# Kernel tuning notes

Hardware: AMD Instinct MI355X
Metric: run time of the kernel (lower is better)

Reference implementation:

```python
import jax, jax.numpy as jnp
import numpy as np

NUM_GRAPHS = 64

def setup_inputs() -> dict:
    key = jax.random.key(0)
    ks = jax.random.split(key, 10)
    N, E, D, V = 100000, 1600000, 64, 30
    node_types = jax.random.randint(ks[0], (N,), 0, V, dtype=jnp.int64 if jax.config.jax_enable_x64 else jnp.int32)
    edge_index = jax.random.randint(ks[1], (2, E), 0, N, dtype=jnp.int32)
    batch = jnp.sort(jax.random.randint(ks[2], (N,), 0, NUM_GRAPHS, dtype=jnp.int32))
    emb_table = jax.random.normal(ks[3], (V, D), dtype=jnp.float32)
    W1 = jax.random.normal(ks[4], (D, D), dtype=jnp.float32) / np.sqrt(D)
    W2 = jax.random.normal(ks[5], (D, D), dtype=jnp.float32) / np.sqrt(D)
    W3 = jax.random.normal(ks[6], (D, D), dtype=jnp.float32) / np.sqrt(D)
    b1 = jnp.zeros((D,), jnp.float32)
    b2 = jnp.zeros((D,), jnp.float32)
    b3 = jnp.zeros((D,), jnp.float32)
    return {"node_types": node_types, "edge_index": edge_index, "batch": batch,
            "emb_table": emb_table, "W1": W1, "b1": b1, "W2": W2, "b2": b2, "W3": W3, "b3": b3}

def _gcn_conv(x, W, b, row, col, norm, N):
    # x' = D^-1/2 (A+I) D^-1/2 (x @ W) + b   (PyG GCNConv semantics)
    h = x @ W
    msg = h[row] * norm[:, None]              # gather + edgewise scale
    out = jax.ops.segment_sum(msg, col, num_segments=N)  # scatter-add at targets
    return out + b

def reference(node_types, edge_index, batch, emb_table, W1, b1, W2, b2, W3, b3):
    N = node_types.shape[0]
    # add self-loops
    loops = jnp.arange(N, dtype=edge_index.dtype)
    row = jnp.concatenate([edge_index[0], loops])
    col = jnp.concatenate([edge_index[1], loops])
    # symmetric normalization on A + I
    deg = jax.ops.segment_sum(jnp.ones_like(col, dtype=jnp.float32), col, num_segments=N)
    dinv = jnp.where(deg > 0, jax.lax.rsqrt(deg), 0.0)
    norm = dinv[row] * dinv[col]
    x = emb_table[node_types]
    x = jax.nn.relu(_gcn_conv(x, W1, b1, row, col, norm, N))
    x = jax.nn.relu(_gcn_conv(x, W2, b2, row, col, norm, N))
    x = _gcn_conv(x, W3, b3, row, col, norm, N)
    # global mean pool over batch segments
    sums = jax.ops.segment_sum(x, batch, num_segments=NUM_GRAPHS)
    cnts = jax.ops.segment_sum(jnp.ones((N,), jnp.float32), batch, num_segments=NUM_GRAPHS)
    pooled = sums / jnp.maximum(cnts, 1.0)[:, None]
    # L2 normalize rows
    return pooled / jnp.linalg.norm(pooled, axis=1, keepdims=True)
```

## Files before the change

kernel.cpp:

```cpp
#include <hip/hip_runtime.h>
#include <hip/hip_fp16.h>

#define DD 64
#define NUM_GRAPHS 64
#define AGG_BLOCKS 2048
#define EB 512
#define BINW 256
#define MAXNB 512
#define EBIN_CAP 6144

typedef _Float16 h2_t __attribute__((ext_vector_type(2)));

__device__ __forceinline__ float fdot2u(unsigned a, unsigned b, float c) {
    return __builtin_amdgcn_fdot2(__builtin_bit_cast(h2_t, a),
                                  __builtin_bit_cast(h2_t, b), c, false);
}

__global__ __launch_bounds__(256) void k_hist(const int* __restrict__ col,
                                              int* __restrict__ H, int E, int NB, int CE) {
    __shared__ int h[MAXNB];
    int eb = blockIdx.x, t = threadIdx.x;
    for (int i = t; i < NB; i += 256) h[i] = 0;
    __syncthreads();
    int e0 = eb * CE, e1 = min(E, e0 + CE);
    for (int e = e0 + t; e < e1; e += 256) atomicAdd(&h[col[e] >> 8], 1);
    __syncthreads();
    for (int i = t; i < NB; i += 256) H[eb * NB + i] = h[i];
}

__global__ __launch_bounds__(256) void k_scanA(int* __restrict__ H,
                                               int* __restrict__ bintot, int NB) {
    __shared__ int s[256];
    int b = blockIdx.x, t = threadIdx.x;
    int i0 = (2 * t) * NB + b, i1 = (2 * t + 1) * NB + b;
    int v0 = H[i0], v1 = H[i1];
    int tot = v0 + v1;
    s[t] = tot;
    __syncthreads();
    for (int off = 1; off < 256; off <<= 1) {
        int tv = (t >= off) ? s[t - off] : 0;
        __syncthreads();
        s[t] += tv;
        __syncthreads();
    }
    int excl = s[t] - tot;
    H[i0] = excl;
    H[i1] = excl + v0;
    if (t == 255) bintot[b] = s[255];
}

__global__ void k_scanB(const int* __restrict__ bintot, int* __restrict__ binstart, int NB) {
    __shared__ int s[512];
    int t = threadIdx.x;
    int v = (t < NB) ? bintot[t] : 0;
    s[t] = v;
    __syncthreads();
    for (int off = 1; off < 512; off <<= 1) {
        int tv = (t >= off) ? s[t - off] : 0;
        __syncthreads();
        s[t] += tv;
        __syncthreads();
    }
    if (t < NB) binstart[t] = s[t] - v;
    if (t == 511) binstart[NB] = s[511];
}

__global__ __launch_bounds__(256) void k_scatbin(const int* __restrict__ row,
                                                 const int* __restrict__ col,
                                                 const int* __restrict__ H,
                                                 const int* __restrict__ binstart,
                                                 unsigned* __restrict__ binned,
                                                 int E, int NB, int CE) {
    __shared__ int off[MAXNB];
    int eb = blockIdx.x, t = threadIdx.x;
    for (int i = t; i < NB; i += 256) off[i] = binstart[i] + H[eb * NB + i];
    __syncthreads();
    int e0 = eb * CE, e1 = min(E, e0 + CE);
    for (int e = e0 + t; e < e1; e += 256) {
        int c = col[e], r = row[e];
        int slot = atomicAdd(&off[c >> 8], 1);
        binned[slot] = ((unsigned)(c & 255) << 24) | (unsigned)r;
    }
}

__global__ __launch_bounds__(256) void k_bincsr(const unsigned* __restrict__ binned,
                                                const int* __restrict__ binstart,
                                                const int* __restrict__ nt,
                                                int* __restrict__ srcidx,
                                                int* __restrict__ rowptr,
                                                float* __restrict__ dinv,
                                                int2* __restrict__ pk, int N, int NB) {
    __shared__ unsigned arr[EBIN_CAP];
    __shared__ int sorted_[EBIN_CAP];
    __shared__ int cnt[BINW];
    __shared__ int base[BINW];
    __shared__ int cursor[BINW];
    int b = blockIdx.x, t = threadIdx.x;
    int s0 = binstart[b], s1 = binstart[b + 1];
    int binsz = s1 - s0;
    if (binsz > EBIN_CAP) binsz = EBIN_CAP;
    cnt[t] = 0;
    for (int i = t; i < binsz; i += 256) arr[i] = binned[s0 + i];
    __syncthreads();
    for (int i = t; i < binsz; i += 256) atomicAdd(&cnt[arr[i] >> 24], 1);
    __syncthreads();
    int v = cnt[t];
    base[t] = v;
    __syncthreads();
    for (int off = 1; off < 256; off <<= 1) {
        int tv = (t >= off) ? base[t - off] : 0;
        __syncthreads();
        base[t] += tv;
        __syncthreads();
    }
    int excl = base[t] - v;
    __syncthreads();
    base[t] = excl;
    cursor[t] = excl;
    __syncthreads();
    for (int i = t; i < binsz; i += 256) {
        unsigned val = arr[i];
        int pos = atomicAdd(&cursor[val >> 24], 1);
        sorted_[pos] = (int)(val & 0xFFFFFF);
    }
    __syncthreads();
    for (int i = t; i < binsz; i += 256) srcidx[s0 + i] = sorted_[i];
    int node = b * BINW + t;
    if (node < N) {
        rowptr[node] = s0 + base[t];
        float di = rsqrtf((float)cnt[t] + 1.0f);
        dinv[node] = di;
        pk[node] = make_int2(nt[node], __float_as_int(di));
    }
    if (b == NB - 1 && t == 0) rowptr[N] = s1;
}

__global__ void k_buildepk(const int* __restrict__ srcidx, const int2* __restrict__ pk,
                           unsigned* __restrict__ epku, int E) {
    int i = blockIdx.x * blockDim.x + threadIdx.x;
    if (i >= E) return;
    int2 p = pk[srcidx[i]];
    epku[i] = ((unsigned)p.x << 16) |
              (unsigned)__half_as_ushort(__float2half(__int_as_float(p.y)));
}

__global__ void k_embW1(const float* __restrict__ emb, const float* __restrict__ W1,
                        float* __restrict__ embW1, int V) {
    __shared__ float er[DD];
    int v = blockIdx.x, j = threadIdx.x;
    er[j] = emb[v * DD + j];
    __syncthreads();
    float acc = 0.0f;
    #pragma unroll
    for (int d = 0; d < DD; ++d) acc += er[d] * W1[d * DD + j];
    embW1[v * DD + j] = acc;
}

__global__ void k_packW(const float* __restrict__ W, unsigned* __restrict__ Wpk) {
    int t = blockIdx.x * blockDim.x + threadIdx.x;
    if (t >= 32 * DD) return;
    int p = t >> 6, j = t & 63;
    __half2 h = __floats2half2_rn(W[(2 * p) * DD + j], W[(2 * p + 1) * DD + j]);
    Wpk[t] = __builtin_bit_cast(unsigned, h);
}

__device__ __forceinline__ void acc_h4(float4& a, uint2 r) {
    float2 f0 = __half22float2(*(const __half2*)&r.x);
    float2 f1 = __half22float2(*(const __half2*)&r.y);
    a.x += f0.x; a.y += f0.y; a.z += f1.x; a.w += f1.y;
}

__device__ __forceinline__ float4 gather_partial_q(const int* __restrict__ srcidx,
                                                   const __half* __restrict__ Hs,
                                                   int s, int e, int g, int l) {
    float4 A = {0,0,0,0}, B = {0,0,0,0}, C = {0,0,0,0}, D = {0,0,0,0};
    int k = s;
    int kend = s + ((e - s) & ~15);
    if (k < kend) {
        uint2 r0 = *(const uint2*)(Hs + (long)srcidx[k + g] * DD + 4 * l);
        uint2 r1 = *(const uint2*)(Hs + (long)srcidx[k + 4 + g] * DD + 4 * l);
        uint2 r2 = *(const uint2*)(Hs + (long)srcidx[k + 8 + g] * DD + 4 * l);
        uint2 r3 = *(const uint2*)(Hs + (long)srcidx[k + 12 + g] * DD + 4 * l);
        k += 16;
        for (; k < kend; k += 16) {
            uint2 n0 = *(const uint2*)(Hs + (long)srcidx[k + g] * DD + 4 * l);
            uint2 n1 = *(const uint2*)(Hs + (long)srcidx[k + 4 + g] * DD + 4 * l);
            uint2 n2 = *(const uint2*)(Hs + (long)srcidx[k + 8 + g] * DD + 4 * l);
            uint2 n3 = *(const uint2*)(Hs + (long)srcidx[k + 12 + g] * DD + 4 * l);
            acc_h4(A, r0); acc_h4(B, r1); acc_h4(C, r2); acc_h4(D, r3);
            r0 = n0; r1 = n1; r2 = n2; r3 = n3;
        }
        acc_h4(A, r0); acc_h4(B, r1); acc_h4(C, r2); acc_h4(D, r3);
    }
    for (; k < e; k += 4) {
        if (k + g < e) {
            uint2 rr = *(const uint2*)(Hs + (long)srcidx[k + g] * DD + 4 * l);
            acc_h4(A, rr);
        }
    }
    A.x += B.x + C.x + D.x; A.y += B.y + C.y + D.y;
    A.z += B.z + C.z + D.z; A.w += B.w + C.w + D.w;
    return A;
}

__device__ __forceinline__ void acc_h8(float4& A, float4& B, uint4 r) {
    float2 f0 = __half22float2(*(const __half2*)&r.x);
    float2 f1 = __half22float2(*(const __half2*)&r.y);
    float2 f2 = __half22float2(*(const __half2*)&r.z);
    float2 f3 = __half22float2(*(const __half2*)&r.w);
    A.x += f0.x; A.y += f0.y; A.z += f1.x; A.w += f1.y;
    B.x += f2.x; B.y += f2.y; B.z += f3.x; B.w += f3.y;
}

__device__ __forceinline__ void gather_sum_8(const int* __restrict__ srcidx,
                                             const __half* __restrict__ Hs,
                                             int s, int e, int g, int l,
                                             float4& A, float4& B) {
    float4 A1 = {0.f, 0.f, 0.f, 0.f}, B1 = {0.f, 0.f, 0.f, 0.f};
    int k = s;
    int kend = s + ((e - s) & ~15);
    if (k < kend) {
        uint4 r0 = *(const uint4*)(Hs + (long)srcidx[k + g] * DD + 8 * l);
        uint4 r1 = *(const uint4*)(Hs + (long)srcidx[k + 8 + g] * DD + 8 * l);
        k += 16;
        for (; k < kend; k += 16) {
            uint4 n0 = *(const uint4*)(Hs + (long)srcidx[k + g] * DD + 8 * l);
            uint4 n1 = *(const uint4*)(Hs + (long)srcidx[k + 8 + g] * DD + 8 * l);
            acc_h8(A, B, r0);
            acc_h8(A1, B1, r1);
            r0 = n0; r1 = n1;
        }
        acc_h8(A, B, r0);
        acc_h8(A1, B1, r1);
    }
    if (k + 8 <= e) {
        uint4 r = *(const uint4*)(Hs + (long)srcidx[k + g] * DD + 8 * l);
        acc_h8(A, B, r);
        k += 8;
    }
    if (k + g < e) {
        uint4 r = *(const uint4*)(Hs + (long)srcidx[k + g] * DD + 8 * l);
        acc_h8(A1, B1, r);
    }
    A.x += A1.x; A.y += A1.y; A.z += A1.z; A.w += A1.w;
    B.x += B1.x; B.y += B1.y; B.z += B1.z; B.w += B1.w;
}

__global__ __launch_bounds__(256, 4) void k_agg1_fused(const int* __restrict__ rowptr,
                                                    const unsigned* __restrict__ epku,
                                                    const int2* __restrict__ pk,
                                                    const float* __restrict__ embW1,
                                                    const float* __restrict__ b1,
                                                    __half* __restrict__ OUT, int N, int V) {
    __shared__ float ew[30 * DD];
    int tid = threadIdx.x;
    for (int k = tid; k < V * DD; k += 256) ew[k] = embW1[k];
    __syncthreads();
    int lane = tid & 63;
    int g = lane >> 4, l = lane & 15;
    float4 bq = *(const float4*)(b1 + 4 * l);
    int wave0 = blockIdx.x * 4 + (tid >> 6);
    int wstride = gridDim.x * 4;
    for (int node = __builtin_amdgcn_readfirstlane(wave0); node < N;
         node += wstride) {
        int s = rowptr[node], e = rowptr[node + 1];
        float4 acc = {0.f, 0.f, 0.f, 0.f};
        int k = s;
        for (; k + 8 <= e; k += 8) {
            unsigned u0 = epku[k + g];
            unsigned u1 = epku[k + 4 + g];
            int t0 = u0 >> 16, t1 = u1 >> 16;
            float d0 = __half2float(__ushort_as_half((unsigned short)(u0 & 0xFFFF)));
            float d1 = __half2float(__ushort_as_half((unsigned short)(u1 & 0xFFFF)));
            float4 w0 = *(const float4*)(ew + t0 * DD + 4 * l);
            float4 w1 = *(const float4*)(ew + t1 * DD + 4 * l);
            acc.x += w0.x * d0 + w1.x * d1;
            acc.y += w0.y * d0 + w1.y * d1;
            acc.z += w0.z * d0 + w1.z * d1;
            acc.w += w0.w * d0 + w1.w * d1;
        }
        if (k + 4 <= e) {
            unsigned u0 = epku[k + g];
            int t0 = u0 >> 16;
            float d0 = __half2float(__ushort_as_half((unsigned short)(u0 & 0xFFFF)));
            float4 w0 = *(const float4*)(ew + t0 * DD + 4 * l);
            acc.x += w0.x * d0; acc.y += w0.y * d0;
            acc.z += w0.z * d0; acc.w += w0.w * d0;
            k += 4;
        }
        if (k + g < e) {
            unsigned u0 = epku[k + g];
            int t0 = u0 >> 16;
            float d0 = __half2float(__ushort_as_half((unsigned short)(u0 & 0xFFFF)));
            float4 w0 = *(const float4*)(ew + t0 * DD + 4 * l);
            acc.x += w0.x * d0; acc.y += w0.y * d0;
            acc.z += w0.z * d0; acc.w += w0.w * d0;
        }
        acc.x += __shfl_xor(acc.x, 16, 64); acc.x += __shfl_xor(acc.x, 32, 64);
        acc.y += __shfl_xor(acc.y, 16, 64); acc.y += __shfl_xor(acc.y, 32, 64);
        acc.z += __shfl_xor(acc.z, 16, 64); acc.z += __shfl_xor(acc.z, 32, 64);
        acc.w += __shfl_xor(acc.w, 16, 64); acc.w += __shfl_xor(acc.w, 32, 64);
        int2 pc = pk[node];
        float dc = __int_as_float(pc.y);
        float4 wc = *(const float4*)(ew + pc.x * DD + 4 * l);
        float4 v;
        v.x = fmaxf((acc.x + wc.x * dc) * dc + bq.x, 0.f) * dc;
        v.y = fmaxf((acc.y + wc.y * dc) * dc + bq.y, 0.f) * dc;
        v.z = fmaxf((acc.z + wc.z * dc) * dc + bq.z, 0.f) * dc;
        v.w = fmaxf((acc.w + wc.w * dc) * dc + bq.w, 0.f) * dc;
        if (g == 0) {
            __half2 h0 = __floats2half2_rn(v.x, v.y);
            __half2 h1 = __floats2half2_rn(v.z, v.w);
            uint2 st;
            st.x = __builtin_bit_cast(unsigned, h0);
            st.y = __builtin_bit_cast(unsigned, h1);
            *(uint2*)(OUT + (long)node * DD + 4 * l) = st;
        }
    }
}

__global__ __launch_bounds__(256, 4) void k_agg2_fused(const int* __restrict__ rowptr,
                                                    const int* __restrict__ srcidx,
                                                    const float* __restrict__ dinv,
                                                    const __half* __restrict__ Hs,
                                                    const float* __restrict__ b2,
                                                    const unsigned* __restrict__ W2pk,
                                                    __half* __restrict__ OUT, int N) {
    int tid = threadIdx.x;
    int lane = tid & 63;
    int g = lane >> 3, l = lane & 7;
    unsigned Wc[32];
    #pragma unroll
    for (int p = 0; p < 32; ++p) Wc[p] = W2pk[p * DD + lane];
    float bl = b2[lane];
    int wstride = gridDim.x * 4;
    int node = __builtin_amdgcn_readfirstlane(blockIdx.x * 4 + (tid >> 6));
    int s = 0, e = 0;
    if (node < N) { s = rowptr[node]; e = rowptr[node + 1]; }
    while (node < N) {
        int nn = node + wstride;
        int ns = 0, ne = 0;
        if (nn < N) { ns = rowptr[nn]; ne = rowptr[nn + 1]; }
        float dc = dinv[node];
        uint4 sr = *(const uint4*)(Hs + (long)node * DD + 8 * l);
        float4 A = {0.f, 0.f, 0.f, 0.f}, B = {0.f, 0.f, 0.f, 0.f};
        gather_sum_8(srcidx, Hs, s, e, g, l, A, B);
        #pragma unroll
        for (int m = 8; m <= 32; m <<= 1) {
            A.x += __shfl_xor(A.x, m, 64); A.y += __shfl_xor(A.y, m, 64);
            A.z += __shfl_xor(A.z, m, 64); A.w += __shfl_xor(A.w, m, 64);
            B.x += __shfl_xor(B.x, m, 64); B.y += __shfl_xor(B.y, m, 64);
            B.z += __shfl_xor(B.z, m, 64); B.w += __shfl_xor(B.w, m, 64);
        }
        float2 s0 = __half22float2(*(const __half2*)&sr.x);
        float2 s1 = __half22float2(*(const __half2*)&sr.y);
        float2 s2 = __half22float2(*(const __half2*)&sr.z);
        float2 s3 = __half22float2(*(const __half2*)&sr.w);
        float t0 = (A.x + s0.x) * dc, t1 = (A.y + s0.y) * dc;
        float t2 = (A.z + s1.x) * dc, t3 = (A.w + s1.y) * dc;
        float t4 = (B.x + s2.x) * dc, t5 = (B.y + s2.y) * dc;
        float t6 = (B.z + s3.x) * dc, t7 = (B.w + s3.y) * dc;
        int vp0 = __builtin_bit_cast(int, __floats2half2_rn(t0, t1));
        int vp1 = __builtin_bit_cast(int, __floats2half2_rn(t2, t3));
        int vp2 = __builtin_bit_cast(int, __floats2half2_rn(t4, t5));
        int vp3 = __builtin_bit_cast(int, __floats2half2_rn(t6, t7));
        float o0 = 0.f, o1 = 0.f, o2 = 0.f, o3 = 0.f;
        #pragma unroll
        for (int p = 0; p < 32; p += 4) {
            o0 = fdot2u((unsigned)__builtin_amdgcn_readlane(vp0, p >> 2), Wc[p + 0], o0);
            o1 = fdot2u((unsigned)__builtin_amdgcn_readlane(vp1, p >> 2), Wc[p + 1], o1);
            o2 = fdot2u((unsigned)__builtin_amdgcn_readlane(vp2, p >> 2), Wc[p + 2], o2);
            o3 = fdot2u((unsigned)__builtin_amdgcn_readlane(vp3, p >> 2), Wc[p + 3], o3);
        }
        float u = (o0 + o1) + (o2 + o3);
        float v2 = fmaxf(u + bl, 0.f);
        OUT[(long)node * DD + lane] = __float2half(v2 * dc);
        node = nn; s = ns; e = ne;
    }
}

__device__ __forceinline__ void flush_pool_q(float4& PA, float* __restrict__ pool,
                                             int gcur, int g, int l) {
    PA.x += __shfl_xor(PA.x, 16, 64); PA.x += __shfl_xor(PA.x, 32, 64);
    PA.y += __shfl_xor(PA.y, 16, 64); PA.y += __shfl_xor(PA.y, 32, 64);
    PA.z += __shfl_xor(PA.z, 16, 64); PA.z += __shfl_xor(PA.z, 32, 64);
    PA.w += __shfl_xor(PA.w, 16, 64); PA.w += __shfl_xor(PA.w, 32, 64);
    if (g == 0) {
        atomicAdd(&pool[gcur * DD + 4 * l + 0], PA.x);
        atomicAdd(&pool[gcur * DD + 4 * l + 1], PA.y);
        atomicAdd(&pool[gcur * DD + 4 * l + 2], PA.z);
        atomicAdd(&pool[gcur * DD + 4 * l + 3], PA.w);
    }
}

__global__ __launch_bounds__(256, 4) void k_agg3_pool(const int* __restrict__ rowptr,
                                                   const int* __restrict__ srcidx,
                                                   const float* __restrict__ dinv,
                                                   const __half* __restrict__ Hs,
                                                   const int* __restrict__ batch,
                                                   float* __restrict__ pool,
                                                   int N, int chunk) {
    int tid = threadIdx.x;
    int lane = tid & 63;
    int g = lane >> 4, l = lane & 15;
    int w = __builtin_amdgcn_readfirstlane(blockIdx.x * 4 + (tid >> 6));
    int start = w * chunk;
    if (start >= N) return;
    int endn = min(N, start + chunk);
    int gcur = batch[start];
    float4 PA = {0.f, 0.f, 0.f, 0.f};
    int s = rowptr[start];
    for (int node = start; node < endn; ++node) {
        int e = rowptr[node + 1];
        float dc = dinv[node];
        int gb = batch[node];
        uint2 sr = *(const uint2*)(Hs + (long)node * DD + 4 * l);
        float4 A = gather_partial_q(srcidx, Hs, s, e, g, l);
        if (g == 0) {
            float2 s0 = __half22float2(*(const __half2*)&sr.x);
            float2 s1 = __half22float2(*(const __half2*)&sr.y);
            A.x += s0.x; A.y += s0.y; A.z += s1.x; A.w += s1.y;
        }
        if (gb != gcur) {
            flush_pool_q(PA, pool, gcur, g, l);
            gcur = gb;
            PA.x = dc * A.x; PA.y = dc * A.y; PA.z = dc * A.z; PA.w = dc * A.w;
        } else {
            PA.x += dc * A.x; PA.y += dc * A.y; PA.z += dc * A.z; PA.w += dc * A.w;
        }
        s = e;
    }
    flush_pool_q(PA, pool, gcur, g, l);
}

__global__ void k_final(const float* __restrict__ pool, const int* __restrict__ batch,
                        const float* __restrict__ W3, const float* __restrict__ b3,
                        float* __restrict__ out, int N) {
    __shared__ float pr[DD];
    int g = blockIdx.x, j = threadIdx.x;
    pr[j] = pool[g * DD + j];
    __syncthreads();
    int lo = 0, hi = N;
    while (lo < hi) { int m = (lo + hi) >> 1; if (batch[m] < g) lo = m + 1; else hi = m; }
    int lo2 = lo; hi = N;
    while (lo2 < hi) { int m = (lo2 + hi) >> 1; if (batch[m] < g + 1) lo2 = m + 1; else hi = m; }
    float cnt = fmaxf((float)(lo2 - lo), 1.0f);
    float acc = 0.0f;
    #pragma unroll
    for (int d = 0; d < DD; ++d) acc += pr[d] * W3[d * DD + j];
    float v = acc / cnt + b3[j];
    float sq = v * v;
    #pragma unroll
    for (int off = 32; off > 0; off >>= 1) sq += __shfl_down(sq, off, 64);
    float nrm = __shfl(sq, 0, 64);
    out[g * DD + j] = v / sqrtf(nrm);
}

extern "C" void kernel_launch(void* const* d_in, const int* in_sizes, int n_in,
                              void* d_out, int out_size, void* d_ws, size_t ws_size,
                              hipStream_t stream) {
    const int*   node_types = (const int*)d_in[0];
    const int*   edge_index = (const int*)d_in[1];
    const int*   batch      = (const int*)d_in[2];
    const float* emb        = (const float*)d_in[3];
    const float* W1 = (const float*)d_in[4];
    const float* b1 = (const float*)d_in[5];
    const float* W2 = (const float*)d_in[6];
    const float* b2 = (const float*)d_in[7];
    const float* W3 = (const float*)d_in[8];
    const float* b3 = (const float*)d_in[9];
    const int N = in_sizes[0];
    const int E = in_sizes[1] / 2;
    const int V = in_sizes[3] / DD;
    const int* row = edge_index;
    const int* col = edge_index + E;
    const long ND = (long)N * DD;
    const int NB = (N + BINW - 1) / BINW;
    const int CE = (E + EB - 1) / EB;

    char* p = (char*)d_ws;
    __half*   hsA     = (__half*)p;       p += ND * sizeof(__half);
    __half*   hsB     = (__half*)p;       p += ND * sizeof(__half);
    int*      srcidx  = (int*)p;          p += (size_t)E * sizeof(int);
    unsigned* epku    = (unsigned*)p;     p += (size_t)E * sizeof(unsigned);
    unsigned* binned  = (unsigned*)p;     p += (size_t)E * sizeof(unsigned);
    int*      H       = (int*)p;          p += (size_t)EB * NB * sizeof(int);
    int*      bintot  = (int*)p;          p += (size_t)(NB + 4) * sizeof(int);
    int*      binstart= (int*)p;          p += (size_t)(NB + 4) * sizeof(int);
    float*    dinv    = (float*)p;        p += (size_t)N * sizeof(float);
    int2*     pk      = (int2*)p;         p += (size_t)N * sizeof(int2);
    int*      rowptr  = (int*)p;          p += (size_t)(N + 4) * sizeof(int);
    float*    pool    = (float*)p;        p += (size_t)NUM_GRAPHS * DD * sizeof(float);
    float*    embW1   = (float*)p;        p += (size_t)V * DD * sizeof(float);
    unsigned* W2pk    = (unsigned*)p;     p += 32 * DD * sizeof(unsigned);

    k_hist<<<EB, 256, 0, stream>>>(col, H, E, NB, CE);
    k_scanA<<<NB, 256, 0, stream>>>(H, bintot, NB);
    k_scanB<<<1, 512, 0, stream>>>(bintot, binstart, NB);
    k_scatbin<<<EB, 256, 0, stream>>>(row, col, H, binstart, binned, E, NB, CE);
    k_bincsr<<<NB, 256, 0, stream>>>(binned, binstart, node_types, srcidx, rowptr,
                                     dinv, pk, N, NB);
    k_buildepk<<<(E + 255) / 256, 256, 0, stream>>>(srcidx, pk, epku, E);

    k_embW1<<<V, DD, 0, stream>>>(emb, W1, embW1, V);
    k_packW<<<8, 256, 0, stream>>>(W2, W2pk);

    k_agg1_fused<<<AGG_BLOCKS, 256, 0, stream>>>(rowptr, epku, pk, embW1, b1,
                                                 hsA, N, V);
    k_agg2_fused<<<AGG_BLOCKS, 256, 0, stream>>>(rowptr, srcidx, dinv, hsA, b2, W2pk,
                                                 hsB, N);
    hipMemsetAsync(pool, 0, (size_t)(NUM_GRAPHS * DD) * sizeof(float), stream);
    const int totalWaves = AGG_BLOCKS * 4;
    const int chunk = (N + totalWaves - 1) / totalWaves;
    k_agg3_pool<<<AGG_BLOCKS, 256, 0, stream>>>(rowptr, srcidx, dinv, hsB, batch,
                                                pool, N, chunk);
    k_final<<<NUM_GRAPHS, DD, 0, stream>>>(pool, batch, W3, b3, (float*)d_out, N);
}
```

Before: 278.9 us.

## Make layer-3 pooling edge-parallel with per-edge batch/dinv packs; prefetch first neighbours

The CSR build now writes a per-edge word packing the target node's graph id and fp16 dinv. It reuses the binned buffer, which each block has already copied to shared memory. Layer-3 aggregation plus pooling becomes an edge-partitioned kernel: each wave walks an even slice of edges, uses wave-uniform checks to batch 16 edges of the same graph, and flushes to the pool on graph changes. Self-loop contributions move to a separate node-parallel kernel, and layers 1 and 2 prefetch the next node's first neighbour indices to hide index-load latency. This aims to balance work and drop rowptr/batch lookups, at the cost of an extra launch, extra per-edge writes in the CSR build, and more pool atomics.

```diff
diff --git a/kernel.cpp b/kernel.cpp
--- a/kernel.cpp
+++ b/kernel.cpp
@@ -15,6 +15,8 @@
     return __builtin_amdgcn_fdot2(__builtin_bit_cast(h2_t, a),
                                   __builtin_bit_cast(h2_t, b), c, false);
 }
+
+#define MDLO(m) __half2float(__ushort_as_half((unsigned short)((m) & 0xFFFF)))
 
 __global__ __launch_bounds__(256) void k_hist(const int* __restrict__ col,
                                               int* __restrict__ H, int E, int NB, int CE) {
@@ -83,18 +85,21 @@
     }
 }
 
-__global__ __launch_bounds__(256) void k_bincsr(const unsigned* __restrict__ binned,
+__global__ __launch_bounds__(256) void k_bincsr(const unsigned* binned,
                                                 const int* __restrict__ binstart,
                                                 const int* __restrict__ nt,
+                                                const int* __restrict__ batch,
                                                 int* __restrict__ srcidx,
                                                 int* __restrict__ rowptr,
                                                 float* __restrict__ dinv,
-                                                int2* __restrict__ pk, int N, int NB) {
+                                                int2* __restrict__ pk,
+                                                unsigned* e3pk, int N, int NB) {
     __shared__ unsigned arr[EBIN_CAP];
     __shared__ int sorted_[EBIN_CAP];
     __shared__ int cnt[BINW];
     __shared__ int base[BINW];
     __shared__ int cursor[BINW];
+    __shared__ unsigned packS[BINW];
     int b = blockIdx.x, t = threadIdx.x;
     int s0 = binstart[b], s1 = binstart[b + 1];
     int binsz = s1 - s0;
@@ -105,6 +110,13 @@
     for (int i = t; i < binsz; i += 256) atomicAdd(&cnt[arr[i] >> 24], 1);
     __syncthreads();
     int v = cnt[t];
+    float di = rsqrtf((float)v + 1.0f);
+    {
+        int nodeT = b * BINW + t;
+        int bt = (nodeT < N) ? batch[nodeT] : 0;
+        packS[t] = ((unsigned)bt << 16) |
+                   (unsigned)__half_as_ushort(__float2half(di));
+    }
     base[t] = v;
     __syncthreads();
     for (int off = 1; off < 256; off <<= 1) {
@@ -120,15 +132,16 @@
     __syncthreads();
     for (int i = t; i < binsz; i += 256) {
         unsigned val = arr[i];
-        int pos = atomicAdd(&cursor[val >> 24], 1);
+        int d = val >> 24;
+        int pos = atomicAdd(&cursor[d], 1);
         sorted_[pos] = (int)(val & 0xFFFFFF);
+        e3pk[s0 + pos] = packS[d];
     }
     __syncthreads();
     for (int i = t; i < binsz; i += 256) srcidx[s0 + i] = sorted_[i];
     int node = b * BINW + t;
     if (node < N) {
         rowptr[node] = s0 + base[t];
-        float di = rsqrtf((float)cnt[t] + 1.0f);
         dinv[node] = di;
         pk[node] = make_int2(nt[node], __float_as_int(di));
     }
@@ -164,45 +177,6 @@
     Wpk[t] = __builtin_bit_cast(unsigned, h);
 }
 
-__device__ __forceinline__ void acc_h4(float4& a, uint2 r) {
-    float2 f0 = __half22float2(*(const __half2*)&r.x);
-    float2 f1 = __half22float2(*(const __half2*)&r.y);
-    a.x += f0.x; a.y += f0.y; a.z += f1.x; a.w += f1.y;
-}
-
-__device__ __forceinline__ float4 gather_partial_q(const int* __restrict__ srcidx,
-                                                   const __half* __restrict__ Hs,
-                                                   int s, int e, int g, int l) {
-    float4 A = {0,0,0,0}, B = {0,0,0,0}, C = {0,0,0,0}, D = {0,0,0,0};
-    int k = s;
-    int kend = s + ((e - s) & ~15);
-    if (k < kend) {
-        uint2 r0 = *(const uint2*)(Hs + (long)srcidx[k + g] * DD + 4 * l);
-        uint2 r1 = *(const uint2*)(Hs + (long)srcidx[k + 4 + g] * DD + 4 * l);
-        uint2 r2 = *(const uint2*)(Hs + (long)srcidx[k + 8 + g] * DD + 4 * l);
-        uint2 r3 = *(const uint2*)(Hs + (long)srcidx[k + 12 + g] * DD + 4 * l);
-        k += 16;
-        for (; k < kend; k += 16) {
-            uint2 n0 = *(const uint2*)(Hs + (long)srcidx[k + g] * DD + 4 * l);
-            uint2 n1 = *(const uint2*)(Hs + (long)srcidx[k + 4 + g] * DD + 4 * l);
-            uint2 n2 = *(const uint2*)(Hs + (long)srcidx[k + 8 + g] * DD + 4 * l);
-            uint2 n3 = *(const uint2*)(Hs + (long)srcidx[k + 12 + g] * DD + 4 * l);
-            acc_h4(A, r0); acc_h4(B, r1); acc_h4(C, r2); acc_h4(D, r3);
-            r0 = n0; r1 = n1; r2 = n2; r3 = n3;
-        }
-        acc_h4(A, r0); acc_h4(B, r1); acc_h4(C, r2); acc_h4(D, r3);
-    }
-    for (; k < e; k += 4) {
-        if (k + g < e) {
-            uint2 rr = *(const uint2*)(Hs + (long)srcidx[k + g] * DD + 4 * l);
-            acc_h4(A, rr);
-        }
-    }
-    A.x += B.x + C.x + D.x; A.y += B.y + C.y + D.y;
-    A.z += B.z + C.z + D.z; A.w += B.w + C.w + D.w;
-    return A;
-}
-
 __device__ __forceinline__ void acc_h8(float4& A, float4& B, uint4 r) {
     float2 f0 = __half22float2(*(const __half2*)&r.x);
     float2 f1 = __half22float2(*(const __half2*)&r.y);
@@ -212,16 +186,16 @@
     B.x += f2.x; B.y += f2.y; B.z += f3.x; B.w += f3.y;
 }
 
-__device__ __forceinline__ void gather_sum_8(const int* __restrict__ srcidx,
-                                             const __half* __restrict__ Hs,
-                                             int s, int e, int g, int l,
-                                             float4& A, float4& B) {
+__device__ __forceinline__ void gather_sum_8p(const int* __restrict__ srcidx,
+                                              const __half* __restrict__ Hs,
+                                              int s, int e, int g, int l,
+                                              float4& A, float4& B, int pi0, int pi1) {
     float4 A1 = {0.f, 0.f, 0.f, 0.f}, B1 = {0.f, 0.f, 0.f, 0.f};
     int k = s;
     int kend = s + ((e - s) & ~15);
     if (k < kend) {
-        uint4 r0 = *(const uint4*)(Hs + (long)srcidx[k + g] * DD + 8 * l);
-        uint4 r1 = *(const uint4*)(Hs + (long)srcidx[k + 8 + g] * DD + 8 * l);
+        uint4 r0 = *(const uint4*)(Hs + (long)pi0 * DD + 8 * l);
+        uint4 r1 = *(const uint4*)(Hs + (long)pi1 * DD + 8 * l);
         k += 16;
         for (; k < kend; k += 16) {
             uint4 n0 = *(const uint4*)(Hs + (long)srcidx[k + g] * DD + 8 * l);
@@ -259,48 +233,51 @@
     int lane = tid & 63;
     int g = lane >> 4, l = lane & 15;
     float4 bq = *(const float4*)(b1 + 4 * l);
-    int wave0 = blockIdx.x * 4 + (tid >> 6);
     int wstride = gridDim.x * 4;
-    for (int node = __builtin_amdgcn_readfirstlane(wave0); node < N;
-         node += wstride) {
-        int s = rowptr[node], e = rowptr[node + 1];
+    int node = __builtin_amdgcn_readfirstlane(blockIdx.x * 4 + (tid >> 6));
+    int s = 0, e = 0;
+    unsigned pu0 = 0, pu1 = 0;
+    if (node < N) {
+        s = rowptr[node]; e = rowptr[node + 1];
+        if (e - s >= 8) { pu0 = epku[s + g]; pu1 = epku[s + 4 + g]; }
+    }
+#define P8(U0, U1) { \
+        unsigned _u0 = (U0), _u1 = (U1); \
+        int _t0 = _u0 >> 16, _t1 = _u1 >> 16; \
+        float _d0 = MDLO(_u0), _d1 = MDLO(_u1); \
+        float4 _w0 = *(const float4*)(ew + _t0 * DD + 4 * l); \
+        float4 _w1 = *(const float4*)(ew + _t1 * DD + 4 * l); \
+        acc.x += _w0.x * _d0 + _w1.x * _d1; \
+        acc.y += _w0.y * _d0 + _w1.y * _d1; \
+        acc.z += _w0.z * _d0 + _w1.z * _d1; \
+        acc.w += _w0.w * _d0 + _w1.w * _d1; }
+#define P4(U0) { \
+        unsigned _u0 = (U0); \
+        int _t0 = _u0 >> 16; \
+        float _d0 = MDLO(_u0); \
+        float4 _w0 = *(const float4*)(ew + _t0 * DD + 4 * l); \
+        acc.x += _w0.x * _d0; acc.y += _w0.y * _d0; \
+        acc.z += _w0.z * _d0; acc.w += _w0.w * _d0; }
+    while (node < N) {
+        int nn = node + wstride;
+        int ns = 0, ne = 0;
+        if (nn < N) { ns = rowptr[nn]; ne = rowptr[nn + 1]; }
+        int2 pc = pk[node];
         float4 acc = {0.f, 0.f, 0.f, 0.f};
         int k = s;
-        for (; k + 8 <= e; k += 8) {
-            unsigned u0 = epku[k + g];
-            unsigned u1 = epku[k + 4 + g];
-            int t0 = u0 >> 16, t1 = u1 >> 16;
-            float d0 = __half2float(__ushort_as_half((unsigned short)(u0 & 0xFFFF)));
-            float d1 = __half2float(__ushort_as_half((unsigned short)(u1 & 0xFFFF)));
-            float4 w0 = *(const float4*)(ew + t0 * DD + 4 * l);
-            float4 w1 = *(const float4*)(ew + t1 * DD + 4 * l);
-            acc.x += w0.x * d0 + w1.x * d1;
-            acc.y += w0.y * d0 + w1.y * d1;
-            acc.z += w0.z * d0 + w1.z * d1;
-            acc.w += w0.w * d0 + w1.w * d1;
-        }
-        if (k + 4 <= e) {
-            unsigned u0 = epku[k + g];
-            int t0 = u0 >> 16;
-            float d0 = __half2float(__ushort_as_half((unsigned short)(u0 & 0xFFFF)));
-            float4 w0 = *(const float4*)(ew + t0 * DD + 4 * l);
-            acc.x += w0.x * d0; acc.y += w0.y * d0;
-            acc.z += w0.z * d0; acc.w += w0.w * d0;
-            k += 4;
-        }
-        if (k + g < e) {
-            unsigned u0 = epku[k + g];
-            int t0 = u0 >> 16;
-            float d0 = __half2float(__ushort_as_half((unsigned short)(u0 & 0xFFFF)));
-            float4 w0 = *(const float4*)(ew + t0 * DD + 4 * l);
-            acc.x += w0.x * d0; acc.y += w0.y * d0;
-            acc.z += w0.z * d0; acc.w += w0.w * d0;
-        }
+        if (k + 8 <= e) {
+            P8(pu0, pu1);
+            k += 8;
+            for (; k + 8 <= e; k += 8) P8(epku[k + g], epku[k + 4 + g]);
+        }
+        if (k + 4 <= e) { P4(epku[k + g]); k += 4; }
+        if (k + g < e)  { P4(epku[k + g]); }
+        unsigned npu0 = 0, npu1 = 0;
+        if (nn < N && ne - ns >= 8) { npu0 = epku[ns + g]; npu1 = epku[ns + 4 + g]; }
         acc.x += __shfl_xor(acc.x, 16, 64); acc.x += __shfl_xor(acc.x, 32, 64);
         acc.y += __shfl_xor(acc.y, 16, 64); acc.y += __shfl_xor(acc.y, 32, 64);
         acc.z += __shfl_xor(acc.z, 16, 64); acc.z += __shfl_xor(acc.z, 32, 64);
         acc.w += __shfl_xor(acc.w, 16, 64); acc.w += __shfl_xor(acc.w, 32, 64);
-        int2 pc = pk[node];
         float dc = __int_as_float(pc.y);
         float4 wc = *(const float4*)(ew + pc.x * DD + 4 * l);
         float4 v;
@@ -316,7 +293,10 @@
             st.y = __builtin_bit_cast(unsigned, h1);
             *(uint2*)(OUT + (long)node * DD + 4 * l) = st;
         }
-    }
+        node = nn; s = ns; e = ne; pu0 = npu0; pu1 = npu1;
+    }
+#undef P8
+#undef P4
 }
 
 __global__ __launch_bounds__(256, 4) void k_agg2_fused(const int* __restrict__ rowptr,
@@ -336,7 +316,11 @@
     int wstride = gridDim.x * 4;
     int node = __builtin_amdgcn_readfirstlane(blockIdx.x * 4 + (tid >> 6));
     int s = 0, e = 0;
-    if (node < N) { s = rowptr[node]; e = rowptr[node + 1]; }
+    int pi0 = 0, pi1 = 0;
+    if (node < N) {
+        s = rowptr[node]; e = rowptr[node + 1];
+        if (e - s >= 16) { pi0 = srcidx[s + g]; pi1 = srcidx[s + 8 + g]; }
+    }
     while (node < N) {
         int nn = node + wstride;
         int ns = 0, ne = 0;
@@ -344,7 +328,9 @@
         float dc = dinv[node];
         uint4 sr = *(const uint4*)(Hs + (long)node * DD + 8 * l);
         float4 A = {0.f, 0.f, 0.f, 0.f}, B = {0.f, 0.f, 0.f, 0.f};
-        gather_sum_8(srcidx, Hs, s, e, g, l, A, B);
+        gather_sum_8p(srcidx, Hs, s, e, g, l, A, B, pi0, pi1);
+        int npi0 = 0, npi1 = 0;
+        if (nn < N && ne - ns >= 16) { npi0 = srcidx[ns + g]; npi1 = srcidx[ns + 8 + g]; }
         #pragma unroll
         for (int m = 8; m <= 32; m <<= 1) {
             A.x += __shfl_xor(A.x, m, 64); A.y += __shfl_xor(A.y, m, 64);
@@ -375,12 +361,13 @@
         float u = (o0 + o1) + (o2 + o3);
         float v2 = fmaxf(u + bl, 0.f);
         OUT[(long)node * DD + lane] = __float2half(v2 * dc);
-        node = nn; s = ns; e = ne;
+        node = nn; s = ns; e = ne; pi0 = npi0; pi1 = npi1;
     }
 }
 
 __device__ __forceinline__ void flush_pool_q(float4& PA, float* __restrict__ pool,
                                              int gcur, int g, int l) {
+    gcur &= (NUM_GRAPHS - 1);
     PA.x += __shfl_xor(PA.x, 16, 64); PA.x += __shfl_xor(PA.x, 32, 64);
     PA.y += __shfl_xor(PA.y, 16, 64); PA.y += __shfl_xor(PA.y, 32, 64);
     PA.z += __shfl_xor(PA.z, 16, 64); PA.z += __shfl_xor(PA.z, 32, 64);
@@ -393,44 +380,125 @@
     }
 }
 
-__global__ __launch_bounds__(256, 4) void k_agg3_pool(const int* __restrict__ rowptr,
-                                                   const int* __restrict__ srcidx,
-                                                   const float* __restrict__ dinv,
+#define ACC_E(PA, R, D) { \
+    float2 _f0 = __half22float2(*(const __half2*)&(R).x); \
+    float2 _f1 = __half22float2(*(const __half2*)&(R).y); \
+    PA.x += (D) * _f0.x; PA.y += (D) * _f0.y; \
+    PA.z += (D) * _f1.x; PA.w += (D) * _f1.y; }
+
+__global__ __launch_bounds__(256, 4) void k_agg3_pool(const int* __restrict__ srcidx,
+                                                   const unsigned* __restrict__ e3pk,
                                                    const __half* __restrict__ Hs,
-                                                   const int* __restrict__ batch,
                                                    float* __restrict__ pool,
-                                                   int N, int chunk) {
+                                                   int E, int ech) {
     int tid = threadIdx.x;
     int lane = tid & 63;
     int g = lane >> 4, l = lane & 15;
+    int w = __builtin_amdgcn_readfirstlane(blockIdx.x * 4 + (tid >> 6));
+    int k = w * ech;
+    if (k >= E) return;
+    int ke = min(E, k + ech);
+    int gcur = (int)(e3pk[k] >> 16);
+    float4 PA = {0.f, 0.f, 0.f, 0.f};
+    unsigned cm0, cm1, cm2, cm3, nm0 = 0, nm1 = 0, nm2 = 0, nm3 = 0;
+    int ci0, ci1, ci2, ci3, ni0 = 0, ni1 = 0, ni2 = 0, ni3 = 0;
+    uint2 cr0 = {0,0}, cr1 = {0,0}, cr2 = {0,0}, cr3 = {0,0};
+    bool have_cur = false, have_next = false;
+    if (k + 16 <= ke) {
+        cm0 = e3pk[k + g];      cm1 = e3pk[k + 4 + g];
+        cm2 = e3pk[k + 8 + g];  cm3 = e3pk[k + 12 + g];
+        ci0 = srcidx[k + g];     ci1 = srcidx[k + 4 + g];
+        ci2 = srcidx[k + 8 + g]; ci3 = srcidx[k + 12 + g];
+        if (__all((int)((cm0 >> 16) == (unsigned)gcur) & (int)((cm1 >> 16) == (unsigned)gcur) &
+                  (int)((cm2 >> 16) == (unsigned)gcur) & (int)((cm3 >> 16) == (unsigned)gcur))) {
+            cr0 = *(const uint2*)(Hs + (long)ci0 * DD + 4 * l);
+            cr1 = *(const uint2*)(Hs + (long)ci1 * DD + 4 * l);
+            cr2 = *(const uint2*)(Hs + (long)ci2 * DD + 4 * l);
+            cr3 = *(const uint2*)(Hs + (long)ci3 * DD + 4 * l);
+            have_cur = true;
+            if (k + 32 <= ke) {
+                nm0 = e3pk[k + 16 + g];  nm1 = e3pk[k + 20 + g];
+                nm2 = e3pk[k + 24 + g];  nm3 = e3pk[k + 28 + g];
+                ni0 = srcidx[k + 16 + g];  ni1 = srcidx[k + 20 + g];
+                ni2 = srcidx[k + 24 + g];  ni3 = srcidx[k + 28 + g];
+                have_next = true;
+            }
+        }
+    }
+    while (have_cur) {
+        bool next_ok = false;
+        uint2 nr0 = {0,0}, nr1 = {0,0}, nr2 = {0,0}, nr3 = {0,0};
+        if (have_next) {
+            next_ok = __all((int)((nm0 >> 16) == (unsigned)gcur) & (int)((nm1 >> 16) == (unsigned)gcur) &
+                            (int)((nm2 >> 16) == (unsigned)gcur) & (int)((nm3 >> 16) == (unsigned)gcur)) != 0;
+            if (next_ok) {
+                nr0 = *(const uint2*)(Hs + (long)ni0 * DD + 4 * l);
+                nr1 = *(const uint2*)(Hs + (long)ni1 * DD + 4 * l);
+                nr2 = *(const uint2*)(Hs + (long)ni2 * DD + 4 * l);
+                nr3 = *(const uint2*)(Hs + (long)ni3 * DD + 4 * l);
+            }
+        }
+        unsigned fm0 = 0, fm1 = 0, fm2 = 0, fm3 = 0;
+        int fi0 = 0, fi1 = 0, fi2 = 0, fi3 = 0;
+        bool have_f = false;
+        if (next_ok && k + 48 <= ke) {
+            fm0 = e3pk[k + 32 + g];  fm1 = e3pk[k + 36 + g];
+            fm2 = e3pk[k + 40 + g];  fm3 = e3pk[k + 44 + g];
+            fi0 = srcidx[k + 32 + g];  fi1 = srcidx[k + 36 + g];
+            fi2 = srcidx[k + 40 + g];  fi3 = srcidx[k + 44 + g];
+            have_f = true;
+        }
+        float d0 = MDLO(cm0), d1 = MDLO(cm1), d2 = MDLO(cm2), d3 = MDLO(cm3);
+        ACC_E(PA, cr0, d0); ACC_E(PA, cr1, d1);
+        ACC_E(PA, cr2, d2); ACC_E(PA, cr3, d3);
+        k += 16;
+        if (!next_ok) break;
+        cm0 = nm0; cm1 = nm1; cm2 = nm2; cm3 = nm3;
+        cr0 = nr0; cr1 = nr1; cr2 = nr2; cr3 = nr3;
+        nm0 = fm0; nm1 = fm1; nm2 = fm2; nm3 = fm3;
+        ni0 = fi0; ni1 = fi1; ni2 = fi2; ni3 = fi3;
+        have_next = have_f;
+    }
+    for (; k < ke; ++k) {
+        unsigned wu = e3pk[k];
+        int gb = (int)(wu >> 16);
+        if (gb != gcur) {
+            flush_pool_q(PA, pool, gcur, g, l);
+            PA.x = 0.f; PA.y = 0.f; PA.z = 0.f; PA.w = 0.f;
+            gcur = gb;
+        }
+        int src = srcidx[k];
+        uint2 rr = *(const uint2*)(Hs + (long)src * DD + 4 * l);
+        if (g == 0) { float d = MDLO(wu); ACC_E(PA, rr, d); }
+    }
+    flush_pool_q(PA, pool, gcur, g, l);
+}
+
+__global__ __launch_bounds__(256, 4) void k_self3(const float* __restrict__ dinv,
+                                               const __half* __restrict__ Hs,
+                                               const int* __restrict__ batch,
+                                               float* __restrict__ pool,
+                                               int N, int chunk) {
+    int tid = threadIdx.x;
+    int lane = tid & 63;
     int w = __builtin_amdgcn_readfirstlane(blockIdx.x * 4 + (tid >> 6));
     int start = w * chunk;
     if (start >= N) return;
     int endn = min(N, start + chunk);
     int gcur = batch[start];
-    float4 PA = {0.f, 0.f, 0.f, 0.f};
-    int s = rowptr[start];
-    for (int node = start; node < endn; ++node) {
-        int e = rowptr[node + 1];
-        float dc = dinv[node];
-        int gb = batch[node];
-        uint2 sr = *(const uint2*)(Hs + (long)node * DD + 4 * l);
-        float4 A = gather_partial_q(srcidx, Hs, s, e, g, l);
-        if (g == 0) {
-            float2 s0 = __half22float2(*(const __half2*)&sr.x);
-            float2 s1 = __half22float2(*(const __half2*)&sr.y);
-            A.x += s0.x; A.y += s0.y; A.z += s1.x; A.w += s1.y;
-        }
+    float acc = 0.f;
+    for (int n = start; n < endn; ++n) {
+        int gb = batch[n];
+        float v = __half2float(Hs[(long)n * DD + lane]);
+        float dc = dinv[n];
         if (gb != gcur) {
-            flush_pool_q(PA, pool, gcur, g, l);
+            atomicAdd(&pool[gcur * DD + lane], acc);
+            acc = 0.f;
             gcur = gb;
-            PA.x = dc * A.x; PA.y = dc * A.y; PA.z = dc * A.z; PA.w = dc * A.w;
-        } else {
-            PA.x += dc * A.x; PA.y += dc * A.y; PA.z += dc * A.z; PA.w += dc * A.w;
-        }
-        s = e;
-    }
-    flush_pool_q(PA, pool, gcur, g, l);
+        }
+        acc += dc * v;
+    }
+    atomicAdd(&pool[gcur * DD + lane], acc);
 }
 
 __global__ void k_final(const float* __restrict__ pool, const int* __restrict__ batch,
@@ -493,13 +561,14 @@
     float*    pool    = (float*)p;        p += (size_t)NUM_GRAPHS * DD * sizeof(float);
     float*    embW1   = (float*)p;        p += (size_t)V * DD * sizeof(float);
     unsigned* W2pk    = (unsigned*)p;     p += 32 * DD * sizeof(unsigned);
+    unsigned* e3pk    = binned;
 
     k_hist<<<EB, 256, 0, stream>>>(col, H, E, NB, CE);
     k_scanA<<<NB, 256, 0, stream>>>(H, bintot, NB);
     k_scanB<<<1, 512, 0, stream>>>(bintot, binstart, NB);
     k_scatbin<<<EB, 256, 0, stream>>>(row, col, H, binstart, binned, E, NB, CE);
-    k_bincsr<<<NB, 256, 0, stream>>>(binned, binstart, node_types, srcidx, rowptr,
-                                     dinv, pk, N, NB);
+    k_bincsr<<<NB, 256, 0, stream>>>(binned, binstart, node_types, batch, srcidx,
+                                     rowptr, dinv, pk, e3pk, N, NB);
     k_buildepk<<<(E + 255) / 256, 256, 0, stream>>>(srcidx, pk, epku, E);
 
     k_embW1<<<V, DD, 0, stream>>>(emb, W1, embW1, V);
@@ -511,8 +580,9 @@
                                                  hsB, N);
     hipMemsetAsync(pool, 0, (size_t)(NUM_GRAPHS * DD) * sizeof(float), stream);
     const int totalWaves = AGG_BLOCKS * 4;
-    const int chunk = (N + totalWaves - 1) / totalWaves;
-    k_agg3_pool<<<AGG_BLOCKS, 256, 0, stream>>>(rowptr, srcidx, dinv, hsB, batch,
-                                                pool, N, chunk);
+    const int ech = (E + totalWaves - 1) / totalWaves;
+    k_agg3_pool<<<AGG_BLOCKS, 256, 0, stream>>>(srcidx, e3pk, hsB, pool, E, ech);
+    const int chunkN = (N + totalWaves - 1) / totalWaves;
+    k_self3<<<AGG_BLOCKS, 256, 0, stream>>>(dinv, hsB, batch, pool, N, chunkN);
     k_final<<<NUM_GRAPHS, DD, 0, stream>>>(pool, batch, W3, b3, (float*)d_out, N);
 }
```

Result: slower. 348.6 us (+25.0%).
